# Kernel optimization log

Hardware: AMD Instinct MI355X
Metric: run time of the kernel (lower is better)

Reference implementation:

```python
import jax, jax.numpy as jnp
import numpy as np

NEG = -1.0e30  # stand-in for -inf, safe under logaddexp in fp32
DEN_SCALE = 1.0


def _ctc_forward(logp, targets, in_lens, tgt_lens):
    """Log-semiring forward (tot score) over the numerator lattice:
    CTC topology composed with the linear target FSA. logp: [B,T,C] (blank=0),
    targets: [B,U] in [1, C-1]. Returns [B] numerator log-scores."""
    B, T, C = logp.shape
    U = targets.shape[1]
    S = 2 * U + 1  # extended label sequence: blank-interleaved
    ext = jnp.zeros((B, S), dtype=jnp.int32).at[:, 1::2].set(targets.astype(jnp.int32))
    # skip transition s-2 -> s allowed only for non-blank, non-repeated labels
    skip_ok = jnp.concatenate(
        [jnp.zeros((B, 2), dtype=bool), (ext[:, 2:] != 0) & (ext[:, 2:] != ext[:, :-2])],
        axis=1,
    )
    emit0 = jnp.take_along_axis(logp[:, 0], ext, axis=1)  # [B,S]
    alpha = jnp.full((B, S), NEG, dtype=logp.dtype)
    alpha = alpha.at[:, 0].set(emit0[:, 0]).at[:, 1].set(emit0[:, 1])
    logp_t = jnp.swapaxes(logp, 0, 1)  # [T,B,C]

    def step(alpha, xs):
        t, lp = xs
        a1 = jnp.concatenate([jnp.full((B, 1), NEG, alpha.dtype), alpha[:, :-1]], axis=1)
        a2 = jnp.concatenate([jnp.full((B, 2), NEG, alpha.dtype), alpha[:, :-2]], axis=1)
        cand = jnp.logaddexp(jnp.logaddexp(alpha, a1), jnp.where(skip_ok, a2, NEG))
        new = cand + jnp.take_along_axis(lp, ext, axis=1)
        alpha = jnp.where((t < in_lens)[:, None], new, alpha)  # freeze past utterance end
        return alpha, None

    alpha, _ = jax.lax.scan(step, alpha, (jnp.arange(1, T), logp_t[1:]))
    last = (2 * tgt_lens).astype(jnp.int32)  # final states: last blank / last label
    a_last = jnp.take_along_axis(alpha, last[:, None], axis=1)[:, 0]
    a_prev = jnp.take_along_axis(alpha, (last - 1)[:, None], axis=1)[:, 0]
    return jnp.logaddexp(a_last, a_prev)


def _den_forward(logp, trans, start, in_lens):
    """Log-semiring forward over the dense denominator graph (bigram token LM):
    states = token classes, transition log-weights trans[C,C]. Returns [B]."""
    B, T, C = logp.shape
    alpha = start[None, :] + logp[:, 0]  # [B,C]
    logp_t = jnp.swapaxes(logp, 0, 1)  # [T,B,C]

    def step(alpha, xs):
        t, lp = xs
        new = jax.nn.logsumexp(alpha[:, :, None] + trans[None], axis=1) + lp
        alpha = jnp.where((t < in_lens)[:, None], new, alpha)
        return alpha, None

    alpha, _ = jax.lax.scan(step, alpha, (jnp.arange(1, T), logp_t[1:]))
    return jax.nn.logsumexp(alpha, axis=1)


def setup_inputs() -> dict:
    key = jax.random.key(0)
    ks = jax.random.split(key, 6)
    B, T, C, U = 32, 2000, 256, 200
    log_probs = jax.nn.log_softmax(jax.random.normal(ks[0], (B, T, C), dtype=jnp.float32), axis=-1)
    targets = jax.random.randint(ks[1], (B, U), 1, C)
    input_lengths = jax.random.randint(ks[2], (B,), T // 2, T + 1)
    target_lengths = jax.random.randint(ks[3], (B,), U // 2, U + 1)
    den_transitions = jax.random.normal(ks[4], (C, C), dtype=jnp.float32) * 0.1
    den_start = jax.random.normal(ks[5], (C,), dtype=jnp.float32) * 0.1
    return {
        "log_probs": log_probs,
        "targets": targets,
        "input_lengths": input_lengths,
        "target_lengths": target_lengths,
        "den_transitions": den_transitions,
        "den_start": den_start,
    }


def reference(log_probs, targets, input_lengths, target_lengths, den_transitions, den_start):
    logp = jax.nn.log_softmax(log_probs, axis=-1)  # idempotent if already normalized
    B, T, C = logp.shape
    U = targets.shape[1]
    in_lens = jnp.clip(input_lengths, 2 * U + 1, T).astype(jnp.int32)
    tgt_lens = jnp.clip(target_lengths, 1, U).astype(jnp.int32)
    tgt = jnp.clip(targets, 1, C - 1)  # blank=0 excluded from targets
    num = _ctc_forward(logp, tgt, in_lens, tgt_lens)
    den = _den_forward(logp, den_transitions, den_start, in_lens)
    tot = num - DEN_SCALE * den  # LF-MMI per-utterance objective
    valid = tot > 0.5 * NEG  # mimic get_tot_objf_and_num_frames -inf filtering
    n = jnp.maximum(jnp.sum(valid), 1)
    return -jnp.sum(jnp.where(valid, tot, 0.0)) / n
```

## Files before the change

### kernel.cpp

```cpp
#include <hip/hip_runtime.h>
#include <stdint.h>
#include <stddef.h>

#define NEGF (-1.0e30f)

typedef __attribute__((ext_vector_type(2))) _Float16 half2_t;
typedef uint32_t u32x16 __attribute__((ext_vector_type(16)));

constexpr int Bn = 32;
constexpr int Tn = 2000;
constexpr int Cn = 256;
constexpr int Un = 200;
constexpr int Sn = 2 * Un + 1;
constexpr float Kn = 4096.0f;

__device__ __forceinline__ float fdot2f(uint32_t a, uint32_t b, float c) {
  half2_t ha = __builtin_bit_cast(half2_t, a);
  half2_t hb = __builtin_bit_cast(half2_t, b);
#if __has_builtin(__builtin_amdgcn_fdot2)
  return __builtin_amdgcn_fdot2(ha, hb, c, false);
#else
  return c + (float)ha.x * (float)hb.x + (float)ha.y * (float)hb.y;
#endif
}

template <int CTRL>
__device__ __forceinline__ float dppf(float x) {
#if __has_builtin(__builtin_amdgcn_update_dpp)
  int xi = __builtin_bit_cast(int, x);
  int y = __builtin_amdgcn_update_dpp(0, xi, CTRL, 0xF, 0xF, false);
  return __builtin_bit_cast(float, y);
#else
  return x;
#endif
}
#define dpp_x1(v) dppf<0xB1>(v)
#define dpp_x2(v) dppf<0x4E>(v)
#define dpp_x7(v) dppf<0x141>(v)

__device__ __forceinline__ uint32_t packe(float a, float b) {
  half2_t h;
  h.x = (_Float16)a;
  h.y = (_Float16)b;
  return __builtin_bit_cast(uint32_t, h);
}

__device__ __forceinline__ float lse3(float a, float b, float c) {
  float m = fmaxf(fmaxf(a, b), c);
  return m + __logf(__expf(a - m) + __expf(b - m) + __expf(c - m));
}

__device__ __forceinline__ int clampi(int v, int lo, int hi) {
  return v < lo ? lo : (v > hi ? hi : v);
}

__global__ __launch_bounds__(256)
__attribute__((amdgpu_waves_per_eu(1, 1)))
void fwd_kernel(
    const float* __restrict__ logp, const int* __restrict__ targets,
    const int* __restrict__ in_lens, const int* __restrict__ tgt_lens,
    const float* __restrict__ trans, const float* __restrict__ start,
    float* __restrict__ ws) {
  const int tid = threadIdx.x;
  const int bid = blockIdx.x;

  if (bid < Bn) {
    const int b = bid;
    const int L = clampi(in_lens[b], Sn, Tn);
    const int q = tid & 7;
    const int u = tid >> 3;
    const int jw = u + 32 * q;

    __shared__ __align__(16) char eaLDS[2 * 8 * 80];
    __shared__ float sred[4];

    const float* trow = trans;
#define EP(c, m) packe(__expf(trow[(32 * q + 2 * (m)) * Cn + (c)]), \
                       __expf(trow[(32 * q + 2 * (m) + 1) * Cn + (c)]))
#define MKCOL(c)                                                          \
  (u32x16){EP(c, 0),  EP(c, 1),  EP(c, 2),  EP(c, 3),  EP(c, 4),          \
           EP(c, 5),  EP(c, 6),  EP(c, 7),  EP(c, 8),  EP(c, 9),          \
           EP(c, 10), EP(c, 11), EP(c, 12), EP(c, 13), EP(c, 14), EP(c, 15)}
    u32x16 E0 = MKCOL(u + 0);
    u32x16 E1 = MKCOL(u + 32);
    u32x16 E2 = MKCOL(u + 64);
    u32x16 E3 = MKCOL(u + 96);
    u32x16 E4 = MKCOL(u + 128);
    u32x16 E5 = MKCOL(u + 160);
    u32x16 E6 = MKCOL(u + 192);
    u32x16 E7 = MKCOL(u + 224);
#undef MKCOL
#undef EP

    const float* lpb = logp + (size_t)b * Tn * Cn;
    const char* rbase0 = eaLDS + 80 * q;
    char* wptr0 = eaLDS + 80 * q + 2 * u;

    float G = -__logf(Kn);
    *(_Float16*)(wptr0) = (_Float16)(Kn * __expf(start[jw] + lpb[jw]));
    float lp_next = lpb[Cn + jw];
    __syncthreads();

    const uint32_t ONE2 = 0x3C003C00u;
    const bool q4 = (q & 4) != 0, q2 = (q & 2) != 0, q1 = (q & 1) != 0;

    for (int t = 1; t < L; ++t) {
      const int pr = (t - 1) & 1, pw = t & 1;
      const float lp_cur = lp_next;
      const int tnext = (t + 1 < L) ? t + 1 : L - 1;
      lp_next = lpb[(size_t)tnext * Cn + jw];
      const float p = __expf(lp_cur);

      const uint4* eap = (const uint4*)(rbase0 + pr * 640);
      float a0 = 0.f, a1 = 0.f, a2 = 0.f, a3 = 0.f;
      float a4 = 0.f, a5 = 0.f, a6 = 0.f, a7 = 0.f;
      half2_t zpk = {(_Float16)0.f, (_Float16)0.f};
#define B2(x) __builtin_bit_cast(half2_t, x)
#define DOT8(idx, ev)               \
  a0 = fdot2f(E0[idx], ev, a0);     \
  a1 = fdot2f(E1[idx], ev, a1);     \
  a2 = fdot2f(E2[idx], ev, a2);     \
  a3 = fdot2f(E3[idx], ev, a3);     \
  a4 = fdot2f(E4[idx], ev, a4);     \
  a5 = fdot2f(E5[idx], ev, a5);     \
  a6 = fdot2f(E6[idx], ev, a6);     \
  a7 = fdot2f(E7[idx], ev, a7);
#define DOTQ(m4)                                                      \
  {                                                                   \
    const uint4 e4 = eap[m4];                                         \
    DOT8(4 * (m4) + 0, e4.x)                                          \
    DOT8(4 * (m4) + 1, e4.y)                                          \
    DOT8(4 * (m4) + 2, e4.z)                                          \
    DOT8(4 * (m4) + 3, e4.w)                                          \
    zpk = zpk + ((B2(e4.x) + B2(e4.y)) + (B2(e4.z) + B2(e4.w)));      \
  }
      DOTQ(0)
      DOTQ(1)
      DOTQ(2)
      DOTQ(3)
#undef DOTQ
#undef DOT8

      float zc = fdot2f(ONE2, __builtin_bit_cast(uint32_t, zpk), 0.f);
      zc += dpp_x1(zc);
      zc += dpp_x2(zc);
      zc += dpp_x7(zc);

      float g, t0, t1, t2, t3, w0, w1, s;
      g = q4 ? a0 : a4;  t0 = (q4 ? a4 : a0) + dpp_x7(g);
      g = q4 ? a1 : a5;  t1 = (q4 ? a5 : a1) + dpp_x7(g);
      g = q4 ? a2 : a6;  t2 = (q4 ? a6 : a2) + dpp_x7(g);
      g = q4 ? a3 : a7;  t3 = (q4 ? a7 : a3) + dpp_x7(g);
      g = q2 ? t0 : t2;  w0 = (q2 ? t2 : t0) + dpp_x2(g);
      g = q2 ? t1 : t3;  w1 = (q2 ? t3 : t1) + dpp_x2(g);
      g = q1 ? w0 : w1;  s  = (q1 ? w1 : w0) + dpp_x1(g);

      const float invZ = Kn * __frcp_rn(zc);
      G -= __logf(invZ);
      *(_Float16*)(wptr0 + pw * 640) = (_Float16)(s * p * invZ);
      __syncthreads();
    }

    {
      const int pL = (L - 1) & 1;
      const char* fb = eaLDS + pL * 640;
      float e = (float)(*(const _Float16*)(fb + 80 * (tid >> 5) + 2 * (tid & 31)));
#pragma unroll
      for (int off = 32; off >= 1; off >>= 1) e += __shfl_xor(e, off, 64);
      const int lane = tid & 63, wid = tid >> 6;
      if (lane == 0) sred[wid] = e;
      __syncthreads();
      if (tid == 0) {
        float ssum = (sred[0] + sred[1]) + (sred[2] + sred[3]);
        ws[Bn + b] = G + __logf(ssum);
      }
    }
  } else {
    const int b = bid - Bn;
    const int L = clampi(in_lens[b], Sn, Tn);
    const int tl = clampi(tgt_lens[b], 1, Un);

    __shared__ float abuf[2][Sn + 3];
    const float* lpb = logp + (size_t)b * Tn * Cn;
    const int* tgtb = targets + b * Un;

    const int s1 = tid;
    const int s2 = tid + 256;
    int e1 = 0, e2 = 0;
    bool k1 = false, k2 = false;
    if (s1 & 1) {
      const int uu = (s1 - 1) >> 1;
      e1 = clampi(tgtb[uu], 1, Cn - 1);
      if (uu > 0) k1 = (e1 != clampi(tgtb[uu - 1], 1, Cn - 1));
    }
    if ((s2 < Sn) && (s2 & 1)) {
      const int uu = (s2 - 1) >> 1;
      e2 = clampi(tgtb[uu], 1, Cn - 1);
      k2 = (e2 != clampi(tgtb[uu - 1], 1, Cn - 1));
    }

    abuf[0][s1 + 2] = (s1 == 0) ? lpb[0] : (s1 == 1 ? lpb[e1] : NEGF);
    if (s2 < Sn) abuf[0][s2 + 2] = NEGF;
    if (tid < 2) { abuf[0][tid] = NEGF; abuf[1][tid] = NEGF; }
    float pe1 = lpb[Cn + e1];
    float pe2 = lpb[Cn + e2];
    __syncthreads();

    int cur = 0;
    for (int t = 1; t < L; ++t) {
      const float em1 = pe1, em2 = pe2;
      const int tnext = (t + 1 < L) ? t + 1 : L - 1;
      pe1 = lpb[(size_t)tnext * Cn + e1];
      pe2 = lpb[(size_t)tnext * Cn + e2];
      const float* A = abuf[cur];
      float* Bv = abuf[cur ^ 1];
      {
        const float x = A[s1 + 2], y = A[s1 + 1];
        const float z = k1 ? A[s1] : NEGF;
        Bv[s1 + 2] = lse3(x, y, z) + em1;
      }
      if (s2 < Sn) {
        const float x = A[s2 + 2], y = A[s2 + 1];
        const float z = k2 ? A[s2] : NEGF;
        Bv[s2 + 2] = lse3(x, y, z) + em2;
      }
      __syncthreads();
      cur ^= 1;
    }
    if (tid == 0) {
      const int l = 2 * tl;
      const float x = abuf[cur][l + 2], y = abuf[cur][l + 1];
      const float m = fmaxf(x, y);
      ws[b] = m + __logf(__expf(x - m) + __expf(y - m));
    }
  }
}

__global__ void finalize_kernel(const float* __restrict__ ws,
                                float* __restrict__ out) {
  const int tid = threadIdx.x;
  float tot = 0.f, cnt = 0.f;
  if (tid < Bn) {
    const float tv = ws[tid] - ws[Bn + tid];
    const bool valid = tv > 0.5f * NEGF;
    tot = valid ? tv : 0.f;
    cnt = valid ? 1.f : 0.f;
  }
#pragma unroll
  for (int off = 32; off >= 1; off >>= 1) {
    tot += __shfl_xor(tot, off, 64);
    cnt += __shfl_xor(cnt, off, 64);
  }
  if (tid == 0) out[0] = -tot / fmaxf(cnt, 1.f);
}

extern "C" void kernel_launch(void* const* d_in, const int* in_sizes, int n_in,
                              void* d_out, int out_size, void* d_ws, size_t ws_size,
                              hipStream_t stream) {
  const float* logp = (const float*)d_in[0];
  const int* targets = (const int*)d_in[1];
  const int* in_lens = (const int*)d_in[2];
  const int* tgt_lens = (const int*)d_in[3];
  const float* trans = (const float*)d_in[4];
  const float* start = (const float*)d_in[5];
  float* ws = (float*)d_ws;
  float* out = (float*)d_out;
  (void)in_sizes; (void)n_in; (void)out_size; (void)ws_size;

  fwd_kernel<<<dim3(2 * Bn), dim3(256), 0, stream>>>(
      logp, targets, in_lens, tgt_lens, trans, start, ws);
  finalize_kernel<<<dim3(1), dim3(64), 0, stream>>>(ws, out);
}
```

Measured before the change: 1.134 ms.

## Split denominator matvec across 512 threads with 16-way row partitioning

Doubles the block to 512 threads, so each denominator thread keeps half as many fp16 transition pairs in registers and does half the dot products per step. The cross-lane reduction gains a level through a ds_swizzle plus DPP row_shr:8, and only even lanes write results. The CTC numerator half now uses one state per thread and prefetches emissions two steps ahead. The intent is a shorter per-timestep serial chain in the latency-bound recurrence, paid for with more barrier participants, an LDS swizzle on the critical path, and dropping the waves_per_eu hint.

```diff
diff --git a/kernel.cpp b/kernel.cpp
--- a/kernel.cpp
+++ b/kernel.cpp
@@ -36,7 +36,13 @@
 }
 #define dpp_x1(v) dppf<0xB1>(v)
 #define dpp_x2(v) dppf<0x4E>(v)
-#define dpp_x7(v) dppf<0x141>(v)
+#define dpp_x8(v) dppf<0x128>(v)
+
+__device__ __forceinline__ float swz4f(float x) {
+  int xi = __builtin_bit_cast(int, x);
+  int y = __builtin_amdgcn_ds_swizzle(xi, 0x101F);
+  return __builtin_bit_cast(float, y);
+}
 
 __device__ __forceinline__ uint32_t packe(float a, float b) {
   half2_t h;
@@ -54,9 +60,7 @@
   return v < lo ? lo : (v > hi ? hi : v);
 }
 
-__global__ __launch_bounds__(256)
-__attribute__((amdgpu_waves_per_eu(1, 1)))
-void fwd_kernel(
+__global__ __launch_bounds__(512) void fwd_kernel(
     const float* __restrict__ logp, const int* __restrict__ targets,
     const int* __restrict__ in_lens, const int* __restrict__ tgt_lens,
     const float* __restrict__ trans, const float* __restrict__ start,
@@ -67,111 +71,111 @@
   if (bid < Bn) {
     const int b = bid;
     const int L = clampi(in_lens[b], Sn, Tn);
-    const int q = tid & 7;
-    const int u = tid >> 3;
-    const int jw = u + 32 * q;
-
-    __shared__ __align__(16) char eaLDS[2 * 8 * 80];
-    __shared__ float sred[4];
-
-    const float* trow = trans;
-#define EP(c, m) packe(__expf(trow[(32 * q + 2 * (m)) * Cn + (c)]), \
-                       __expf(trow[(32 * q + 2 * (m) + 1) * Cn + (c)]))
-#define MKCOL(c)                                                          \
-  (u32x16){EP(c, 0),  EP(c, 1),  EP(c, 2),  EP(c, 3),  EP(c, 4),          \
-           EP(c, 5),  EP(c, 6),  EP(c, 7),  EP(c, 8),  EP(c, 9),          \
-           EP(c, 10), EP(c, 11), EP(c, 12), EP(c, 13), EP(c, 14), EP(c, 15)}
-    u32x16 E0 = MKCOL(u + 0);
-    u32x16 E1 = MKCOL(u + 32);
-    u32x16 E2 = MKCOL(u + 64);
-    u32x16 E3 = MKCOL(u + 96);
-    u32x16 E4 = MKCOL(u + 128);
-    u32x16 E5 = MKCOL(u + 160);
-    u32x16 E6 = MKCOL(u + 192);
-    u32x16 E7 = MKCOL(u + 224);
-#undef MKCOL
-#undef EP
+    const int q = tid & 15;
+    const int u = tid >> 4;
+    const int b3 = (q >> 3) & 1, b2 = (q >> 2) & 1, b1 = (q >> 1) & 1;
+    const int kown = 4 * b3 + 2 * b2 + b1;
+    const int jown = u + 32 * kown;
+
+    __shared__ __align__(16) char eaLDS[2 * 768];
+    __shared__ float sred[8];
+
+#define EPAIR(k, m)                                                   \
+  packe(__expf(trans[(16 * q + 2 * (m)) * Cn + (u + 32 * (k))]),      \
+        __expf(trans[(16 * q + 2 * (m) + 1) * Cn + (u + 32 * (k))]))
+#define COL8(k)                                                       \
+  EPAIR(k, 0), EPAIR(k, 1), EPAIR(k, 2), EPAIR(k, 3),                 \
+  EPAIR(k, 4), EPAIR(k, 5), EPAIR(k, 6), EPAIR(k, 7)
+    u32x16 EV0 = (u32x16){COL8(0), COL8(1)};
+    u32x16 EV1 = (u32x16){COL8(2), COL8(3)};
+    u32x16 EV2 = (u32x16){COL8(4), COL8(5)};
+    u32x16 EV3 = (u32x16){COL8(6), COL8(7)};
+#undef COL8
+#undef EPAIR
 
     const float* lpb = logp + (size_t)b * Tn * Cn;
-    const char* rbase0 = eaLDS + 80 * q;
-    char* wptr0 = eaLDS + 80 * q + 2 * u;
 
     float G = -__logf(Kn);
-    *(_Float16*)(wptr0) = (_Float16)(Kn * __expf(start[jw] + lpb[jw]));
-    float lp_next = lpb[Cn + jw];
+    if (tid < Cn) {
+      *(_Float16*)(eaLDS + 48 * (tid >> 4) + 2 * (tid & 15)) =
+          (_Float16)(Kn * __expf(start[tid] + lpb[tid]));
+    }
+    float p_cur = __expf(lpb[Cn + jown]);
+    float lp_mid = lpb[2 * Cn + jown];
     __syncthreads();
 
     const uint32_t ONE2 = 0x3C003C00u;
-    const bool q4 = (q & 4) != 0, q2 = (q & 2) != 0, q1 = (q & 1) != 0;
+    const char* rchunk = eaLDS + 48 * q;
+    char* wslot = eaLDS + 48 * (jown >> 4) + 2 * (jown & 15);
 
     for (int t = 1; t < L; ++t) {
       const int pr = (t - 1) & 1, pw = t & 1;
-      const float lp_cur = lp_next;
-      const int tnext = (t + 1 < L) ? t + 1 : L - 1;
-      lp_next = lpb[(size_t)tnext * Cn + jw];
-      const float p = __expf(lp_cur);
-
-      const uint4* eap = (const uint4*)(rbase0 + pr * 640);
-      float a0 = 0.f, a1 = 0.f, a2 = 0.f, a3 = 0.f;
-      float a4 = 0.f, a5 = 0.f, a6 = 0.f, a7 = 0.f;
-      half2_t zpk = {(_Float16)0.f, (_Float16)0.f};
-#define B2(x) __builtin_bit_cast(half2_t, x)
-#define DOT8(idx, ev)               \
-  a0 = fdot2f(E0[idx], ev, a0);     \
-  a1 = fdot2f(E1[idx], ev, a1);     \
-  a2 = fdot2f(E2[idx], ev, a2);     \
-  a3 = fdot2f(E3[idx], ev, a3);     \
-  a4 = fdot2f(E4[idx], ev, a4);     \
-  a5 = fdot2f(E5[idx], ev, a5);     \
-  a6 = fdot2f(E6[idx], ev, a6);     \
-  a7 = fdot2f(E7[idx], ev, a7);
-#define DOTQ(m4)                                                      \
-  {                                                                   \
-    const uint4 e4 = eap[m4];                                         \
-    DOT8(4 * (m4) + 0, e4.x)                                          \
-    DOT8(4 * (m4) + 1, e4.y)                                          \
-    DOT8(4 * (m4) + 2, e4.z)                                          \
-    DOT8(4 * (m4) + 3, e4.w)                                          \
-    zpk = zpk + ((B2(e4.x) + B2(e4.y)) + (B2(e4.z) + B2(e4.w)));      \
-  }
-      DOTQ(0)
-      DOTQ(1)
-      DOTQ(2)
-      DOTQ(3)
-#undef DOTQ
-#undef DOT8
-
-      float zc = fdot2f(ONE2, __builtin_bit_cast(uint32_t, zpk), 0.f);
+
+      const uint4* rb = (const uint4*)(rchunk + pr * 768);
+      const uint4 r0 = rb[0], r1 = rb[1];
+
+      half2_t zp = (__builtin_bit_cast(half2_t, r0.x) + __builtin_bit_cast(half2_t, r0.y)) +
+                   (__builtin_bit_cast(half2_t, r0.z) + __builtin_bit_cast(half2_t, r0.w));
+      half2_t zq = (__builtin_bit_cast(half2_t, r1.x) + __builtin_bit_cast(half2_t, r1.y)) +
+                   (__builtin_bit_cast(half2_t, r1.z) + __builtin_bit_cast(half2_t, r1.w));
+      float zc = fdot2f(ONE2, __builtin_bit_cast(uint32_t, zp + zq), 0.f);
       zc += dpp_x1(zc);
       zc += dpp_x2(zc);
-      zc += dpp_x7(zc);
-
-      float g, t0, t1, t2, t3, w0, w1, s;
-      g = q4 ? a0 : a4;  t0 = (q4 ? a4 : a0) + dpp_x7(g);
-      g = q4 ? a1 : a5;  t1 = (q4 ? a5 : a1) + dpp_x7(g);
-      g = q4 ? a2 : a6;  t2 = (q4 ? a6 : a2) + dpp_x7(g);
-      g = q4 ? a3 : a7;  t3 = (q4 ? a7 : a3) + dpp_x7(g);
-      g = q2 ? t0 : t2;  w0 = (q2 ? t2 : t0) + dpp_x2(g);
-      g = q2 ? t1 : t3;  w1 = (q2 ? t3 : t1) + dpp_x2(g);
-      g = q1 ? w0 : w1;  s  = (q1 ? w1 : w0) + dpp_x1(g);
-
+      zc += swz4f(zc);
+      zc += dpp_x8(zc);
       const float invZ = Kn * __frcp_rn(zc);
+      const float pm = p_cur * invZ;
+
+      float c0 = 0.f, c1 = 0.f, c2 = 0.f, c3 = 0.f;
+      float c4 = 0.f, c5 = 0.f, c6 = 0.f, c7 = 0.f;
+#define DCOL(cv, V, base)                  \
+  cv = fdot2f(V[(base) + 0], r0.x, cv);    \
+  cv = fdot2f(V[(base) + 1], r0.y, cv);    \
+  cv = fdot2f(V[(base) + 2], r0.z, cv);    \
+  cv = fdot2f(V[(base) + 3], r0.w, cv);    \
+  cv = fdot2f(V[(base) + 4], r1.x, cv);    \
+  cv = fdot2f(V[(base) + 5], r1.y, cv);    \
+  cv = fdot2f(V[(base) + 6], r1.z, cv);    \
+  cv = fdot2f(V[(base) + 7], r1.w, cv);
+      DCOL(c0, EV0, 0) DCOL(c1, EV0, 8)
+      DCOL(c2, EV1, 0) DCOL(c3, EV1, 8)
+      DCOL(c4, EV2, 0) DCOL(c5, EV2, 8)
+      DCOL(c6, EV3, 0) DCOL(c7, EV3, 8)
+#undef DCOL
+
+      float g, t0, t1, t2, t3, u0, u1, v0;
+      g = b3 ? c0 : c4;  t0 = (b3 ? c4 : c0) + dpp_x8(g);
+      g = b3 ? c1 : c5;  t1 = (b3 ? c5 : c1) + dpp_x8(g);
+      g = b3 ? c2 : c6;  t2 = (b3 ? c6 : c2) + dpp_x8(g);
+      g = b3 ? c3 : c7;  t3 = (b3 ? c7 : c3) + dpp_x8(g);
+      g = b2 ? t0 : t2;  u0 = (b2 ? t2 : t0) + swz4f(g);
+      g = b2 ? t1 : t3;  u1 = (b2 ? t3 : t1) + swz4f(g);
+      g = b1 ? u0 : u1;  v0 = (b1 ? u1 : u0) + dpp_x2(g);
+      const float s = v0 + dpp_x1(v0);
+
+      if ((q & 1) == 0) *(_Float16*)(wslot + pw * 768) = (_Float16)(s * pm);
       G -= __logf(invZ);
-      *(_Float16*)(wptr0 + pw * 640) = (_Float16)(s * p * invZ);
+
+      p_cur = __expf(lp_mid);
+      const int tf = (t + 2 < L) ? t + 2 : L - 1;
+      lp_mid = lpb[(size_t)tf * Cn + jown];
       __syncthreads();
     }
 
     {
       const int pL = (L - 1) & 1;
-      const char* fb = eaLDS + pL * 640;
-      float e = (float)(*(const _Float16*)(fb + 80 * (tid >> 5) + 2 * (tid & 31)));
+      float e = 0.f;
+      if (tid < Cn)
+        e = (float)(*(const _Float16*)(eaLDS + pL * 768 + 48 * (tid >> 4) +
+                                       2 * (tid & 15)));
 #pragma unroll
       for (int off = 32; off >= 1; off >>= 1) e += __shfl_xor(e, off, 64);
       const int lane = tid & 63, wid = tid >> 6;
       if (lane == 0) sred[wid] = e;
       __syncthreads();
       if (tid == 0) {
-        float ssum = (sred[0] + sred[1]) + (sred[2] + sred[3]);
+        float ssum = ((sred[0] + sred[1]) + (sred[2] + sred[3])) +
+                     ((sred[4] + sred[5]) + (sred[6] + sred[7]));
         ws[Bn + b] = G + __logf(ssum);
       }
     }
@@ -184,46 +188,33 @@
     const float* lpb = logp + (size_t)b * Tn * Cn;
     const int* tgtb = targets + b * Un;
 
-    const int s1 = tid;
-    const int s2 = tid + 256;
-    int e1 = 0, e2 = 0;
-    bool k1 = false, k2 = false;
-    if (s1 & 1) {
-      const int uu = (s1 - 1) >> 1;
-      e1 = clampi(tgtb[uu], 1, Cn - 1);
-      if (uu > 0) k1 = (e1 != clampi(tgtb[uu - 1], 1, Cn - 1));
-    }
-    if ((s2 < Sn) && (s2 & 1)) {
-      const int uu = (s2 - 1) >> 1;
-      e2 = clampi(tgtb[uu], 1, Cn - 1);
-      k2 = (e2 != clampi(tgtb[uu - 1], 1, Cn - 1));
-    }
-
-    abuf[0][s1 + 2] = (s1 == 0) ? lpb[0] : (s1 == 1 ? lpb[e1] : NEGF);
-    if (s2 < Sn) abuf[0][s2 + 2] = NEGF;
+    const int s = tid;
+    const bool act = (s < Sn);
+    int e = 0;
+    bool k = false;
+    if (act && (s & 1)) {
+      const int uu = (s - 1) >> 1;
+      e = clampi(tgtb[uu], 1, Cn - 1);
+      if (uu > 0) k = (e != clampi(tgtb[uu - 1], 1, Cn - 1));
+    }
+
+    if (act) abuf[0][s + 2] = (s == 0) ? lpb[0] : (s == 1 ? lpb[e] : NEGF);
     if (tid < 2) { abuf[0][tid] = NEGF; abuf[1][tid] = NEGF; }
-    float pe1 = lpb[Cn + e1];
-    float pe2 = lpb[Cn + e2];
+    float em_cur = lpb[Cn + e];
+    float em_mid = lpb[2 * Cn + e];
     __syncthreads();
 
     int cur = 0;
     for (int t = 1; t < L; ++t) {
-      const float em1 = pe1, em2 = pe2;
-      const int tnext = (t + 1 < L) ? t + 1 : L - 1;
-      pe1 = lpb[(size_t)tnext * Cn + e1];
-      pe2 = lpb[(size_t)tnext * Cn + e2];
       const float* A = abuf[cur];
-      float* Bv = abuf[cur ^ 1];
-      {
-        const float x = A[s1 + 2], y = A[s1 + 1];
-        const float z = k1 ? A[s1] : NEGF;
-        Bv[s1 + 2] = lse3(x, y, z) + em1;
+      if (act) {
+        const float x = A[s + 2], y = A[s + 1];
+        const float z = k ? A[s] : NEGF;
+        abuf[cur ^ 1][s + 2] = lse3(x, y, z) + em_cur;
       }
-      if (s2 < Sn) {
-        const float x = A[s2 + 2], y = A[s2 + 1];
-        const float z = k2 ? A[s2] : NEGF;
-        Bv[s2 + 2] = lse3(x, y, z) + em2;
-      }
+      em_cur = em_mid;
+      const int tf = (t + 2 < L) ? t + 2 : L - 1;
+      em_mid = lpb[(size_t)tf * Cn + e];
       __syncthreads();
       cur ^= 1;
     }
@@ -267,7 +258,7 @@
   float* out = (float*)d_out;
   (void)in_sizes; (void)n_in; (void)out_size; (void)ws_size;
 
-  fwd_kernel<<<dim3(2 * Bn), dim3(256), 0, stream>>>(
+  fwd_kernel<<<dim3(2 * Bn), dim3(512), 0, stream>>>(
       logp, targets, in_lens, tgt_lens, trans, start, ws);
   finalize_kernel<<<dim3(1), dim3(64), 0, stream>>>(ws, out);
 }
```

Result: slower. 1.392 ms (+22.8%).
